# Performance work log

Measured on AMD Instinct MI355X. Metric: run time of the kernel, lower is better.

## Reference

```python
import jax, jax.numpy as jnp
import numpy as np

N_LEVELS = 16  # 2**4, bit = 4 in QuantLinear


def _sum_to(g, shape):
    # reduce grad g to broadcast shape `shape`
    extra = g.ndim - len(shape)
    if extra:
        g = g.sum(axis=tuple(range(extra)))
    axes = tuple(i for i, (gs, s) in enumerate(zip(g.shape, shape)) if s == 1 and gs != 1)
    if axes:
        g = g.sum(axis=axes, keepdims=True)
    return g.reshape(shape)


@jax.custom_vjp
def ste_round(x):
    return jnp.round(x)

def _r_fwd(x):
    return jnp.round(x), None

def _r_bwd(_, g):
    return (g,)

ste_round.defvjp(_r_fwd, _r_bwd)


@jax.custom_vjp
def dclip(x, lo, hi):
    return jnp.clip(x, lo, hi)

def _c_fwd(x, lo, hi):
    return jnp.clip(x, lo, hi), (x, lo, hi)

def _c_bwd(res, g):
    x, lo, hi = res
    gx = jnp.where((x < lo) | (x > hi), 0.0, g)
    glo = _sum_to(jnp.where(x > lo, 0.0, g), lo.shape)
    ghi = _sum_to(jnp.where(x < hi, 0.0, g), hi.shape)
    return gx, glo, ghi

dclip.defvjp(_c_fwd, _c_bwd)


def fake_quant(x, lb, ub):
    # UniformQuantizer.forward
    delta = (ub - lb) / (N_LEVELS - 1)
    x_cut = dclip(x, lb, ub)
    x_int = ste_round((x_cut - lb) / delta)
    return x_int * delta + lb


def setup_inputs() -> dict:
    key = jax.random.key(0)
    k0, k1, k2 = jax.random.split(key, 3)
    B, S, Din, Dout = 4, 4096, 1024, 3072
    x = jax.random.normal(k0, (B, S, Din), jnp.float32)
    weight = jax.random.normal(k1, (Dout, Din), jnp.float32) * 0.02
    bias = jax.random.normal(k2, (Dout,), jnp.float32) * 0.01
    # calibrated per-tensor activation bounds, per-output-channel weight bounds
    in_lb = jnp.full((1,), -2.5, jnp.float32)
    in_ub = jnp.full((1,), 2.5, jnp.float32)
    w_ub = jnp.max(jnp.abs(weight), axis=1, keepdims=True)  # (Dout, 1)
    w_lb = -w_ub
    return {"x": x, "weight": weight, "bias": bias,
            "in_lb": in_lb, "in_ub": in_ub, "w_lb": w_lb, "w_ub": w_ub}


def reference(x, weight, bias, in_lb, in_ub, w_lb, w_ub):
    qx = fake_quant(x, in_lb, in_ub)        # [B,S,Din]
    qw = fake_quant(weight, w_lb, w_ub)     # [Dout,Din]
    return jnp.einsum('bsi,oi->bso', qx, qw) + bias
```

## Files before the change

kernel.cpp:

```cpp
#include <hip/hip_runtime.h>

typedef int i32x4 __attribute__((ext_vector_type(4)));
typedef unsigned char u8x8 __attribute__((ext_vector_type(8)));


__global__ __launch_bounds__(512) void quant_i8_fused(
    const float* __restrict__ x, unsigned char* __restrict__ qx,
    float* __restrict__ Sx, const float* __restrict__ xlb,
    const float* __restrict__ xub, const float* __restrict__ w,
    unsigned char* __restrict__ qw, float* __restrict__ Sw,
    const float* __restrict__ wlb, const float* __restrict__ wub,
    int nxblocks) {
  const int tid = threadIdx.x;
  const int rloc = tid >> 7;
  const bool is_x = (int)blockIdx.x < nxblocks;
  const int rb = is_x ? blockIdx.x : blockIdx.x - nxblocks;
  const int row = rb * 4 + rloc;

  const float* src = is_x ? x : w;
  unsigned char* dst = is_x ? qx : qw;
  float* Sdst = is_x ? Sx : Sw;
  const float lb = is_x ? xlb[0] : wlb[row];
  const float ub = is_x ? xub[0] : wub[row];
  const float delta = (ub - lb) / 15.0f;

  const size_t base = (size_t)row * 1024 + (tid & 127) * 8;
  const float4* p = reinterpret_cast<const float4*>(src + base);
  float4 v0 = p[0], v1 = p[1];
  float vv[8] = {v0.x, v0.y, v0.z, v0.w, v1.x, v1.y, v1.z, v1.w};
  int s = 0;
  u8x8 o;
#pragma unroll
  for (int j = 0; j < 8; ++j) {
    float t = fminf(fmaxf(vv[j], lb), ub);
    int k = (int)rintf((t - lb) / delta);
    s += k;
    o[j] = (unsigned char)k;
  }
  *reinterpret_cast<u8x8*>(dst + base) = o;

#pragma unroll
  for (int d = 32; d > 0; d >>= 1) s += __shfl_down(s, d);
  __shared__ int wsum[8];
  if ((tid & 63) == 0) wsum[tid >> 6] = s;
  __syncthreads();
  if (tid < 4) Sdst[rb * 4 + tid] = (float)(wsum[2 * tid] + wsum[2 * tid + 1]);
}


__device__ __forceinline__ void gload_lds16(const unsigned char* g, unsigned char* l) {
  __builtin_amdgcn_global_load_lds(
      (const __attribute__((address_space(1))) unsigned int*)g,
      (__attribute__((address_space(3))) unsigned int*)l, 16, 0, 0);
}

#define SWZ(o) ((o) ^ ((((o) >> 7) & 3) << 4))

__global__ __launch_bounds__(512, 2) void gemm_i8_kernel(
    const unsigned char* __restrict__ A, const unsigned char* __restrict__ B,
    const float* __restrict__ bias, const float* __restrict__ Sx,
    const float* __restrict__ Sw, const float* __restrict__ wlb,
    const float* __restrict__ wub, const float* __restrict__ xlb,
    const float* __restrict__ xub, float* __restrict__ C, int M, int N) {
  const int K = 1024;
  const int NKT = 16;
  __shared__ unsigned char lds[3][24576];

  const int tid = threadIdx.x;
  const int w = tid >> 6, l = tid & 63;
  const int wm = w >> 1, wn = w & 1;

  int bid = blockIdx.x;
  { const int cpx = gridDim.x >> 3; bid = (bid & 7) * cpx + (bid >> 3); }
  const int ntn = N >> 7;
  const int tm = bid / ntn, tn = bid % ntn;

  const unsigned char* gA = A + (size_t)tm * 256 * K;
  const unsigned char* gB = B + (size_t)tn * 128 * K;

  const int p0 = tid * 16, p1 = 8192 + tid * 16, pB = tid * 16;
  const int o0 = SWZ(p0), o1 = SWZ(p1), oB = SWZ(pB);
  const unsigned char* sA0 = gA + (size_t)(o0 >> 6) * K + (o0 & 63);
  const unsigned char* sA1 = gA + (size_t)(o1 >> 6) * K + (o1 & 63);
  const unsigned char* sB0 = gB + (size_t)(oB >> 6) * K + (oB & 63);

  const int lroff = (l & 15) * 64 + (((l >> 4) * 16) ^ (((l >> 1) & 3) << 4));

#define STAGE_A(SB, KOFF) do {                                           \
    unsigned char* Rb_ = &lds[SB][0];                                    \
    gload_lds16(sA0 + (KOFF), Rb_ + p0);                                 \
    gload_lds16(sA1 + (KOFF), Rb_ + p1);                                 \
  } while (0)
#define STAGE_B(SB, KOFF) do {                                           \
    gload_lds16(sB0 + (KOFF), &lds[SB][16384] + pB);                     \
  } while (0)

#define RD_A(RB, F)  (*(const i32x4*)(&lds[RB][0]     + wm * 4096 + (F) * 1024 + lroff))
#define RD_B(RB, NN) (*(const i32x4*)(&lds[RB][16384] + wn * 4096 + (NN) * 1024 + lroff))

#define BAR __builtin_amdgcn_s_barrier()
#define LGKM0 do { asm volatile("s_waitcnt lgkmcnt(0)" ::: "memory");    \
                   __builtin_amdgcn_sched_barrier(0); } while (0)
#define VMC3 asm volatile("s_waitcnt vmcnt(3)" ::: "memory")

  i32x4 acc[4][4] = {};
  i32x4 av0, av1, av2, av3, bv[4];

#define MFMA_HALF(A0, A1, MH) do {                                       \
    __builtin_amdgcn_s_setprio(1);                                       \
    _Pragma("unroll") for (int nn = 0; nn < 4; ++nn)                     \
      acc[(MH) * 2 + 0][nn] = __builtin_amdgcn_mfma_i32_16x16x64_i8(     \
          A0, bv[nn], acc[(MH) * 2 + 0][nn], 0, 0, 0);                   \
    _Pragma("unroll") for (int nn = 0; nn < 4; ++nn)                     \
      acc[(MH) * 2 + 1][nn] = __builtin_amdgcn_mfma_i32_16x16x64_i8(     \
          A1, bv[nn], acc[(MH) * 2 + 1][nn], 0, 0, 0);                   \
    __builtin_amdgcn_s_setprio(0);                                       \
  } while (0)

  STAGE_A(0, 0); STAGE_B(0, 0);
  STAGE_A(1, 64); STAGE_B(1, 64);
  VMC3; BAR;

#pragma unroll
  for (int t = 0; t < NKT; ++t) {
    const int rb = t % 3, sb = (t + 2) % 3;
    const int koff = (t + 2 < NKT ? (t + 2) : 0) << 6;
    av0 = RD_A(rb, 0); av1 = RD_A(rb, 1);
#pragma unroll
    for (int nn = 0; nn < 4; ++nn) bv[nn] = RD_B(rb, nn);
    STAGE_A(sb, koff);
    BAR; LGKM0;
    MFMA_HALF(av0, av1, 0);
    BAR;
    av2 = RD_A(rb, 2); av3 = RD_A(rb, 3);
    STAGE_B(sb, koff);
    VMC3;
    BAR; LGKM0;
    MFMA_HALF(av2, av3, 1);
    BAR;
  }

  const float lbx = xlb[0];
  const float dx = (xub[0] - lbx) / 15.0f;
  const int rq = (l >> 4) * 4;
  const int cn = l & 15;
  const int mb = tm * 256 + wm * 64;
  const int nb = tn * 128 + wn * 64;

  float sxr[4][4];
#pragma unroll
  for (int m = 0; m < 4; ++m) {
    const int r0 = mb + m * 16 + rq;
#pragma unroll
    for (int j = 0; j < 4; ++j) sxr[m][j] = Sx[r0 + j];
  }
#pragma unroll
  for (int n = 0; n < 4; ++n) {
    const int col = nb + n * 16 + cn;
    const float wl = wlb[col], wu = wub[col];
    const float dw = (wu - wl) / 15.0f;
    const float c1 = dx * dw;
    const float c2 = dx * wl;
    const float c3 = lbx * dw * Sw[col] + 1024.0f * lbx * wl + bias[col];
#pragma unroll
    for (int m = 0; m < 4; ++m) {
      float* cp = C + (size_t)(mb + m * 16 + rq) * N + col;
      __builtin_nontemporal_store(c1 * (float)acc[m][n][0] + c2 * sxr[m][0] + c3, cp);
      __builtin_nontemporal_store(c1 * (float)acc[m][n][1] + c2 * sxr[m][1] + c3, cp + (size_t)N);
      __builtin_nontemporal_store(c1 * (float)acc[m][n][2] + c2 * sxr[m][2] + c3, cp + (size_t)2 * N);
      __builtin_nontemporal_store(c1 * (float)acc[m][n][3] + c2 * sxr[m][3] + c3, cp + (size_t)3 * N);
    }
  }
  asm volatile("s_waitcnt vmcnt(0)" ::: "memory");
#undef STAGE_A
#undef STAGE_B
#undef RD_A
#undef RD_B
#undef BAR
#undef LGKM0
#undef VMC3
#undef MFMA_HALF
}

extern "C" void kernel_launch(void* const* d_in, const int* in_sizes, int n_in,
                              void* d_out, int out_size, void* d_ws, size_t ws_size,
                              hipStream_t stream) {
  const float* x     = (const float*)d_in[0];
  const float* wgt   = (const float*)d_in[1];
  const float* bias  = (const float*)d_in[2];
  const float* in_lb = (const float*)d_in[3];
  const float* in_ub = (const float*)d_in[4];
  const float* w_lb  = (const float*)d_in[5];
  const float* w_ub  = (const float*)d_in[6];

  const int Dout = in_sizes[2];
  const int Din  = in_sizes[1] / Dout;
  const int M    = in_sizes[0] / Din;

  unsigned char* qx = (unsigned char*)d_ws;
  unsigned char* qw = qx + (size_t)M * Din;
  float* Sx = (float*)(qw + (size_t)Dout * Din);
  float* Sw = Sx + M;

  const int nxb = M / 4;
  quant_i8_fused<<<nxb + Dout / 4, 512, 0, stream>>>(
      x, qx, Sx, in_lb, in_ub, wgt, qw, Sw, w_lb, w_ub, nxb);

  dim3 grid((M / 256) * (Dout / 128));
  gemm_i8_kernel<<<grid, 512, 0, stream>>>(qx, qw, bias, Sx, Sw, w_lb, w_ub,
                                           in_lb, in_ub, (float*)d_out, M, Dout);
}
```

Measured before the change: 94.66 us.

## Shrink GEMM tile to 128x128 with 4 waves and load B directly into registers

The int8 GEMM moves from a 256x128 tile with 8 waves to a 128x128 tile with 4 waves and launch bounds of 3 blocks per CU. Only A is still staged through LDS in a triple buffer. Each wave now loads its B fragments straight from global memory into registers, double-buffered one k-step ahead. The goal is to cut LDS traffic and footprint and to simplify the per-k-step barrier schedule, in exchange for more grid blocks, redundant global reads of B across waves and tiles, and less A reuse per block.

Result: slower. 138.8 us (+46.7%).

```diff
diff --git a/kernel.cpp b/kernel.cpp
--- a/kernel.cpp
+++ b/kernel.cpp
@@ -2,7 +2,6 @@
 
 typedef int i32x4 __attribute__((ext_vector_type(4)));
 typedef unsigned char u8x8 __attribute__((ext_vector_type(8)));
-
 
 __global__ __launch_bounds__(512) void quant_i8_fused(
     const float* __restrict__ x, unsigned char* __restrict__ qx,
@@ -56,15 +55,14 @@
 
 #define SWZ(o) ((o) ^ ((((o) >> 7) & 3) << 4))
 
-__global__ __launch_bounds__(512, 2) void gemm_i8_kernel(
+__global__ __launch_bounds__(256, 3) void gemm_i8_kernel(
     const unsigned char* __restrict__ A, const unsigned char* __restrict__ B,
     const float* __restrict__ bias, const float* __restrict__ Sx,
     const float* __restrict__ Sw, const float* __restrict__ wlb,
     const float* __restrict__ wub, const float* __restrict__ xlb,
     const float* __restrict__ xub, float* __restrict__ C, int M, int N) {
   const int K = 1024;
-  const int NKT = 16;
-  __shared__ unsigned char lds[3][24576];
+  __shared__ unsigned char lds[3][8192];
 
   const int tid = threadIdx.x;
   const int w = tid >> 6, l = tid & 63;
@@ -75,76 +73,101 @@
   const int ntn = N >> 7;
   const int tm = bid / ntn, tn = bid % ntn;
 
-  const unsigned char* gA = A + (size_t)tm * 256 * K;
+  const unsigned char* gA = A + (size_t)tm * 128 * K;
   const unsigned char* gB = B + (size_t)tn * 128 * K;
 
-  const int p0 = tid * 16, p1 = 8192 + tid * 16, pB = tid * 16;
-  const int o0 = SWZ(p0), o1 = SWZ(p1), oB = SWZ(pB);
+  const int p0 = tid * 16, p1 = 4096 + tid * 16;
+  const int o0 = SWZ(p0), o1 = SWZ(p1);
   const unsigned char* sA0 = gA + (size_t)(o0 >> 6) * K + (o0 & 63);
   const unsigned char* sA1 = gA + (size_t)(o1 >> 6) * K + (o1 & 63);
-  const unsigned char* sB0 = gB + (size_t)(oB >> 6) * K + (oB & 63);
 
   const int lroff = (l & 15) * 64 + (((l >> 4) * 16) ^ (((l >> 1) & 3) << 4));
 
-#define STAGE_A(SB, KOFF) do {                                           \
+  const unsigned char* gB0 = gB + (size_t)(wn * 64 + (l & 15)) * K + (l >> 4) * 16;
+
+#define STAGE(SB, KOFF) do {                                             \
     unsigned char* Rb_ = &lds[SB][0];                                    \
     gload_lds16(sA0 + (KOFF), Rb_ + p0);                                 \
     gload_lds16(sA1 + (KOFF), Rb_ + p1);                                 \
   } while (0)
-#define STAGE_B(SB, KOFF) do {                                           \
-    gload_lds16(sB0 + (KOFF), &lds[SB][16384] + pB);                     \
+
+#define RD_A(RB, F) (*(const i32x4*)(&lds[RB][0] + wm * 4096 + (F) * 1024 + lroff))
+
+#define LOADB(D0, D1, D2, D3, T) do {                                    \
+    const int ko_ = ((T) < 16 ? (T) : 0) * 64;                           \
+    D0 = *(const i32x4*)(gB0 + ko_);                                     \
+    D1 = *(const i32x4*)(gB0 + 16 * 1024 + ko_);                         \
+    D2 = *(const i32x4*)(gB0 + 32 * 1024 + ko_);                         \
+    D3 = *(const i32x4*)(gB0 + 48 * 1024 + ko_);                         \
   } while (0)
 
-#define RD_A(RB, F)  (*(const i32x4*)(&lds[RB][0]     + wm * 4096 + (F) * 1024 + lroff))
-#define RD_B(RB, NN) (*(const i32x4*)(&lds[RB][16384] + wn * 4096 + (NN) * 1024 + lroff))
-
-#define BAR __builtin_amdgcn_s_barrier()
-#define LGKM0 do { asm volatile("s_waitcnt lgkmcnt(0)" ::: "memory");    \
-                   __builtin_amdgcn_sched_barrier(0); } while (0)
-#define VMC3 asm volatile("s_waitcnt vmcnt(3)" ::: "memory")
+#define SCB __builtin_amdgcn_sched_barrier(0)
+#define VMC0 do { asm volatile("s_waitcnt vmcnt(0)" ::: "memory"); SCB; } while (0)
+#define BARS do { __builtin_amdgcn_s_barrier(); SCB; } while (0)
 
   i32x4 acc[4][4] = {};
-  i32x4 av0, av1, av2, av3, bv[4];
-
-#define MFMA_HALF(A0, A1, MH) do {                                       \
+  i32x4 av0, av1, av2, av3;
+  i32x4 bc0, bc1, bc2, bc3, bn0, bn1, bn2, bn3;
+
+#define MF(AV, BV, CC) __builtin_amdgcn_mfma_i32_16x16x64_i8(AV, BV, CC, 0, 0, 0)
+
+#define TILE(T, C0, C1, C2, C3, N0, N1, N2, N3) do {                     \
+    av0 = RD_A((T) % 3, 0); av1 = RD_A((T) % 3, 1);                      \
+    av2 = RD_A((T) % 3, 2); av3 = RD_A((T) % 3, 3);                      \
+    LOADB(N0, N1, N2, N3, (T) + 1);                                      \
+    SCB;                                                                 \
     __builtin_amdgcn_s_setprio(1);                                       \
-    _Pragma("unroll") for (int nn = 0; nn < 4; ++nn)                     \
-      acc[(MH) * 2 + 0][nn] = __builtin_amdgcn_mfma_i32_16x16x64_i8(     \
-          A0, bv[nn], acc[(MH) * 2 + 0][nn], 0, 0, 0);                   \
-    _Pragma("unroll") for (int nn = 0; nn < 4; ++nn)                     \
-      acc[(MH) * 2 + 1][nn] = __builtin_amdgcn_mfma_i32_16x16x64_i8(     \
-          A1, bv[nn], acc[(MH) * 2 + 1][nn], 0, 0, 0);                   \
+    acc[0][0] = MF(av0, C0, acc[0][0]);                                  \
+    acc[0][1] = MF(av0, C1, acc[0][1]);                                  \
+    acc[0][2] = MF(av0, C2, acc[0][2]);                                  \
+    acc[0][3] = MF(av0, C3, acc[0][3]);                                  \
+    acc[1][0] = MF(av1, C0, acc[1][0]);                                  \
+    acc[1][1] = MF(av1, C1, acc[1][1]);                                  \
+    acc[1][2] = MF(av1, C2, acc[1][2]);                                  \
+    acc[1][3] = MF(av1, C3, acc[1][3]);                                  \
+    acc[2][0] = MF(av2, C0, acc[2][0]);                                  \
+    acc[2][1] = MF(av2, C1, acc[2][1]);                                  \
+    acc[2][2] = MF(av2, C2, acc[2][2]);                                  \
+    acc[2][3] = MF(av2, C3, acc[2][3]);                                  \
+    acc[3][0] = MF(av3, C0, acc[3][0]);                                  \
+    acc[3][1] = MF(av3, C1, acc[3][1]);                                  \
+    acc[3][2] = MF(av3, C2, acc[3][2]);                                  \
+    acc[3][3] = MF(av3, C3, acc[3][3]);                                  \
     __builtin_amdgcn_s_setprio(0);                                       \
+    VMC0; BARS;                                                          \
+    STAGE(((T) + 2) % 3, ((T) + 2 < 16 ? (T) + 2 : 0) * 64);             \
+    SCB;                                                                 \
   } while (0)
 
-  STAGE_A(0, 0); STAGE_B(0, 0);
-  STAGE_A(1, 64); STAGE_B(1, 64);
-  VMC3; BAR;
-
-#pragma unroll
-  for (int t = 0; t < NKT; ++t) {
-    const int rb = t % 3, sb = (t + 2) % 3;
-    const int koff = (t + 2 < NKT ? (t + 2) : 0) << 6;
-    av0 = RD_A(rb, 0); av1 = RD_A(rb, 1);
-#pragma unroll
-    for (int nn = 0; nn < 4; ++nn) bv[nn] = RD_B(rb, nn);
-    STAGE_A(sb, koff);
-    BAR; LGKM0;
-    MFMA_HALF(av0, av1, 0);
-    BAR;
-    av2 = RD_A(rb, 2); av3 = RD_A(rb, 3);
-    STAGE_B(sb, koff);
-    VMC3;
-    BAR; LGKM0;
-    MFMA_HALF(av2, av3, 1);
-    BAR;
-  }
+  STAGE(0, 0);
+  STAGE(1, 64);
+  LOADB(bc0, bc1, bc2, bc3, 0);
+  VMC0; BARS;
+
+  TILE(0,  bc0, bc1, bc2, bc3, bn0, bn1, bn2, bn3);
+  TILE(1,  bn0, bn1, bn2, bn3, bc0, bc1, bc2, bc3);
+  TILE(2,  bc0, bc1, bc2, bc3, bn0, bn1, bn2, bn3);
+  TILE(3,  bn0, bn1, bn2, bn3, bc0, bc1, bc2, bc3);
+  TILE(4,  bc0, bc1, bc2, bc3, bn0, bn1, bn2, bn3);
+  TILE(5,  bn0, bn1, bn2, bn3, bc0, bc1, bc2, bc3);
+  TILE(6,  bc0, bc1, bc2, bc3, bn0, bn1, bn2, bn3);
+  TILE(7,  bn0, bn1, bn2, bn3, bc0, bc1, bc2, bc3);
+  TILE(8,  bc0, bc1, bc2, bc3, bn0, bn1, bn2, bn3);
+  TILE(9,  bn0, bn1, bn2, bn3, bc0, bc1, bc2, bc3);
+  TILE(10, bc0, bc1, bc2, bc3, bn0, bn1, bn2, bn3);
+  TILE(11, bn0, bn1, bn2, bn3, bc0, bc1, bc2, bc3);
+  TILE(12, bc0, bc1, bc2, bc3, bn0, bn1, bn2, bn3);
+  TILE(13, bn0, bn1, bn2, bn3, bc0, bc1, bc2, bc3);
+  TILE(14, bc0, bc1, bc2, bc3, bn0, bn1, bn2, bn3);
+  TILE(15, bn0, bn1, bn2, bn3, bc0, bc1, bc2, bc3);
+
+  VMC0;
 
   const float lbx = xlb[0];
   const float dx = (xub[0] - lbx) / 15.0f;
   const int rq = (l >> 4) * 4;
   const int cn = l & 15;
-  const int mb = tm * 256 + wm * 64;
+  const int mb = tm * 128 + wm * 64;
   const int nb = tn * 128 + wn * 64;
 
   float sxr[4][4];
@@ -171,15 +194,14 @@
       __builtin_nontemporal_store(c1 * (float)acc[m][n][3] + c2 * sxr[m][3] + c3, cp + (size_t)3 * N);
     }
   }
-  asm volatile("s_waitcnt vmcnt(0)" ::: "memory");
-#undef STAGE_A
-#undef STAGE_B
+#undef STAGE
 #undef RD_A
-#undef RD_B
-#undef BAR
-#undef LGKM0
-#undef VMC3
-#undef MFMA_HALF
+#undef LOADB
+#undef SCB
+#undef VMC0
+#undef BARS
+#undef MF
+#undef TILE
 }
 
 extern "C" void kernel_launch(void* const* d_in, const int* in_sizes, int n_in,
@@ -206,7 +228,7 @@
   quant_i8_fused<<<nxb + Dout / 4, 512, 0, stream>>>(
       x, qx, Sx, in_lb, in_ub, wgt, qw, Sw, w_lb, w_ub, nxb);
 
-  dim3 grid((M / 256) * (Dout / 128));
-  gemm_i8_kernel<<<grid, 512, 0, stream>>>(qx, qw, bias, Sx, Sw, w_lb, w_ub,
+  dim3 grid((M / 128) * (Dout / 128));
+  gemm_i8_kernel<<<grid, 256, 0, stream>>>(qx, qw, bias, Sx, Sw, w_lb, w_ub,
                                            in_lb, in_ub, (float*)d_out, M, Dout);
 }
```

## Enlarge GEMM tile to 256x256 with double-buffered LDS pipeline

Applied to the files above, without the earlier changes.

The int8 GEMM block tile grows from 256x128 to 256x256, with each wave computing 128x64 outputs (32 accumulators) so every loaded A/B fragment is reused more. The LDS pipeline moves from three stages with split half-tiles and several barriers to two full-tile buffers, with one vmcnt(0) wait and one barrier per K step. The aim is to raise arithmetic intensity and cut synchronisation. In exchange, register pressure rises (128 accumulator VGPRs), the grid has half as many blocks, and global loads now overlap only one tile of compute.

Result: slower. 111.0 us (+17.3%).

```diff
diff --git a/kernel.cpp b/kernel.cpp
--- a/kernel.cpp
+++ b/kernel.cpp
@@ -2,7 +2,6 @@
 
 typedef int i32x4 __attribute__((ext_vector_type(4)));
 typedef unsigned char u8x8 __attribute__((ext_vector_type(8)));
-
 
 __global__ __launch_bounds__(512) void quant_i8_fused(
     const float* __restrict__ x, unsigned char* __restrict__ qx,
@@ -64,25 +63,26 @@
     const float* __restrict__ xub, float* __restrict__ C, int M, int N) {
   const int K = 1024;
   const int NKT = 16;
-  __shared__ unsigned char lds[3][24576];
+  __shared__ unsigned char lds[2][32768];
 
   const int tid = threadIdx.x;
   const int w = tid >> 6, l = tid & 63;
-  const int wm = w >> 1, wn = w & 1;
+  const int wm = w >> 2, wn = w & 3;
 
   int bid = blockIdx.x;
   { const int cpx = gridDim.x >> 3; bid = (bid & 7) * cpx + (bid >> 3); }
-  const int ntn = N >> 7;
+  const int ntn = N >> 8;
   const int tm = bid / ntn, tn = bid % ntn;
 
   const unsigned char* gA = A + (size_t)tm * 256 * K;
-  const unsigned char* gB = B + (size_t)tn * 128 * K;
-
-  const int p0 = tid * 16, p1 = 8192 + tid * 16, pB = tid * 16;
-  const int o0 = SWZ(p0), o1 = SWZ(p1), oB = SWZ(pB);
+  const unsigned char* gB = B + (size_t)tn * 256 * K;
+
+  const int p0 = tid * 16, p1 = 8192 + tid * 16;
+  const int o0 = SWZ(p0), o1 = SWZ(p1);
   const unsigned char* sA0 = gA + (size_t)(o0 >> 6) * K + (o0 & 63);
   const unsigned char* sA1 = gA + (size_t)(o1 >> 6) * K + (o1 & 63);
-  const unsigned char* sB0 = gB + (size_t)(oB >> 6) * K + (oB & 63);
+  const unsigned char* sB0 = gB + (size_t)(o0 >> 6) * K + (o0 & 63);
+  const unsigned char* sB1 = gB + (size_t)(o1 >> 6) * K + (o1 & 63);
 
   const int lroff = (l & 15) * 64 + (((l >> 4) * 16) ^ (((l >> 1) & 3) << 4));
 
@@ -92,68 +92,69 @@
     gload_lds16(sA1 + (KOFF), Rb_ + p1);                                 \
   } while (0)
 #define STAGE_B(SB, KOFF) do {                                           \
-    gload_lds16(sB0 + (KOFF), &lds[SB][16384] + pB);                     \
-  } while (0)
-
-#define RD_A(RB, F)  (*(const i32x4*)(&lds[RB][0]     + wm * 4096 + (F) * 1024 + lroff))
+    unsigned char* Rb_ = &lds[SB][16384];                                \
+    gload_lds16(sB0 + (KOFF), Rb_ + p0);                                 \
+    gload_lds16(sB1 + (KOFF), Rb_ + p1);                                 \
+  } while (0)
+
+#define RD_A(RB, F)  (*(const i32x4*)(&lds[RB][0]     + wm * 8192 + (F) * 1024 + lroff))
 #define RD_B(RB, NN) (*(const i32x4*)(&lds[RB][16384] + wn * 4096 + (NN) * 1024 + lroff))
 
-#define BAR __builtin_amdgcn_s_barrier()
+#define BARS do { __builtin_amdgcn_s_barrier();                          \
+                  __builtin_amdgcn_sched_barrier(0); } while (0)
 #define LGKM0 do { asm volatile("s_waitcnt lgkmcnt(0)" ::: "memory");    \
                    __builtin_amdgcn_sched_barrier(0); } while (0)
-#define VMC3 asm volatile("s_waitcnt vmcnt(3)" ::: "memory")
-
-  i32x4 acc[4][4] = {};
-  i32x4 av0, av1, av2, av3, bv[4];
-
-#define MFMA_HALF(A0, A1, MH) do {                                       \
+#define VMC0 do { asm volatile("s_waitcnt vmcnt(0)" ::: "memory");       \
+                  __builtin_amdgcn_sched_barrier(0); } while (0)
+
+  i32x4 acc[8][4] = {};
+  i32x4 av0, av1, av2, av3, av4, av5, av6, av7, bv0, bv1, bv2, bv3;
+
+#define MF(AV, BV, CC) __builtin_amdgcn_mfma_i32_16x16x64_i8(AV, BV, CC, 0, 0, 0)
+
+#define MROW(MI, AV) do {                                                \
+    acc[MI][0] = MF(AV, bv0, acc[MI][0]);                                \
+    acc[MI][1] = MF(AV, bv1, acc[MI][1]);                                \
+    acc[MI][2] = MF(AV, bv2, acc[MI][2]);                                \
+    acc[MI][3] = MF(AV, bv3, acc[MI][3]);                                \
+  } while (0)
+
+#define TILE(T) do {                                                     \
+    const int rb_ = (T) & 1, sb_ = ((T) + 1) & 1;                        \
+    const int ko_ = ((T) + 1 < NKT ? (T) + 1 : 0) << 6;                  \
+    av0 = RD_A(rb_, 0); av1 = RD_A(rb_, 1);                              \
+    av2 = RD_A(rb_, 2); av3 = RD_A(rb_, 3);                              \
+    bv0 = RD_B(rb_, 0); bv1 = RD_B(rb_, 1);                              \
+    bv2 = RD_B(rb_, 2); bv3 = RD_B(rb_, 3);                              \
+    STAGE_A(sb_, ko_);                                                   \
+    STAGE_B(sb_, ko_);                                                   \
+    LGKM0;                                                               \
     __builtin_amdgcn_s_setprio(1);                                       \
-    _Pragma("unroll") for (int nn = 0; nn < 4; ++nn)                     \
-      acc[(MH) * 2 + 0][nn] = __builtin_amdgcn_mfma_i32_16x16x64_i8(     \
-          A0, bv[nn], acc[(MH) * 2 + 0][nn], 0, 0, 0);                   \
-    _Pragma("unroll") for (int nn = 0; nn < 4; ++nn)                     \
-      acc[(MH) * 2 + 1][nn] = __builtin_amdgcn_mfma_i32_16x16x64_i8(     \
-          A1, bv[nn], acc[(MH) * 2 + 1][nn], 0, 0, 0);                   \
+    MROW(0, av0); MROW(1, av1); MROW(2, av2); MROW(3, av3);              \
     __builtin_amdgcn_s_setprio(0);                                       \
-  } while (0)
-
-  STAGE_A(0, 0); STAGE_B(0, 0);
-  STAGE_A(1, 64); STAGE_B(1, 64);
-  VMC3; BAR;
-
-#pragma unroll
-  for (int t = 0; t < NKT; ++t) {
-    const int rb = t % 3, sb = (t + 2) % 3;
-    const int koff = (t + 2 < NKT ? (t + 2) : 0) << 6;
-    av0 = RD_A(rb, 0); av1 = RD_A(rb, 1);
-#pragma unroll
-    for (int nn = 0; nn < 4; ++nn) bv[nn] = RD_B(rb, nn);
-    STAGE_A(sb, koff);
-    BAR; LGKM0;
-    MFMA_HALF(av0, av1, 0);
-    BAR;
-    av2 = RD_A(rb, 2); av3 = RD_A(rb, 3);
-    STAGE_B(sb, koff);
-    VMC3;
-    BAR; LGKM0;
-    MFMA_HALF(av2, av3, 1);
-    BAR;
-  }
+    av4 = RD_A(rb_, 4); av5 = RD_A(rb_, 5);                              \
+    av6 = RD_A(rb_, 6); av7 = RD_A(rb_, 7);                              \
+    LGKM0;                                                               \
+    __builtin_amdgcn_s_setprio(1);                                       \
+    MROW(4, av4); MROW(5, av5); MROW(6, av6); MROW(7, av7);              \
+    __builtin_amdgcn_s_setprio(0);                                       \
+    VMC0; BARS;                                                          \
+  } while (0)
+
+  STAGE_A(0, 0);
+  STAGE_B(0, 0);
+  VMC0; BARS;
+
+#pragma unroll
+  for (int t = 0; t < NKT; ++t) TILE(t);
 
   const float lbx = xlb[0];
   const float dx = (xub[0] - lbx) / 15.0f;
   const int rq = (l >> 4) * 4;
   const int cn = l & 15;
-  const int mb = tm * 256 + wm * 64;
-  const int nb = tn * 128 + wn * 64;
-
-  float sxr[4][4];
-#pragma unroll
-  for (int m = 0; m < 4; ++m) {
-    const int r0 = mb + m * 16 + rq;
-#pragma unroll
-    for (int j = 0; j < 4; ++j) sxr[m][j] = Sx[r0 + j];
-  }
+  const int mb = tm * 256 + wm * 128;
+  const int nb = tn * 256 + wn * 64;
+
 #pragma unroll
   for (int n = 0; n < 4; ++n) {
     const int col = nb + n * 16 + cn;
@@ -163,23 +164,25 @@
     const float c2 = dx * wl;
     const float c3 = lbx * dw * Sw[col] + 1024.0f * lbx * wl + bias[col];
 #pragma unroll
-    for (int m = 0; m < 4; ++m) {
-      float* cp = C + (size_t)(mb + m * 16 + rq) * N + col;
-      __builtin_nontemporal_store(c1 * (float)acc[m][n][0] + c2 * sxr[m][0] + c3, cp);
-      __builtin_nontemporal_store(c1 * (float)acc[m][n][1] + c2 * sxr[m][1] + c3, cp + (size_t)N);
-      __builtin_nontemporal_store(c1 * (float)acc[m][n][2] + c2 * sxr[m][2] + c3, cp + (size_t)2 * N);
-      __builtin_nontemporal_store(c1 * (float)acc[m][n][3] + c2 * sxr[m][3] + c3, cp + (size_t)3 * N);
+    for (int m = 0; m < 8; ++m) {
+      const int r0 = mb + m * 16 + rq;
+      float* cp = C + (size_t)r0 * N + col;
+      __builtin_nontemporal_store(c1 * (float)acc[m][n][0] + c2 * Sx[r0 + 0] + c3, cp);
+      __builtin_nontemporal_store(c1 * (float)acc[m][n][1] + c2 * Sx[r0 + 1] + c3, cp + (size_t)N);
+      __builtin_nontemporal_store(c1 * (float)acc[m][n][2] + c2 * Sx[r0 + 2] + c3, cp + (size_t)2 * N);
+      __builtin_nontemporal_store(c1 * (float)acc[m][n][3] + c2 * Sx[r0 + 3] + c3, cp + (size_t)3 * N);
     }
   }
-  asm volatile("s_waitcnt vmcnt(0)" ::: "memory");
 #undef STAGE_A
 #undef STAGE_B
 #undef RD_A
 #undef RD_B
-#undef BAR
+#undef BARS
 #undef LGKM0
-#undef VMC3
-#undef MFMA_HALF
+#undef VMC0
+#undef MF
+#undef MROW
+#undef TILE
 }
 
 extern "C" void kernel_launch(void* const* d_in, const int* in_sizes, int n_in,
@@ -206,7 +209,7 @@
   quant_i8_fused<<<nxb + Dout / 4, 512, 0, stream>>>(
       x, qx, Sx, in_lb, in_ub, wgt, qw, Sw, w_lb, w_ub, nxb);
 
-  dim3 grid((M / 256) * (Dout / 128));
+  dim3 grid((M / 256) * (Dout / 256));
   gemm_i8_kernel<<<grid, 512, 0, stream>>>(qx, qw, bias, Sx, Sw, w_lb, w_ub,
                                            in_lb, in_ub, (float*)d_out, M, Dout);
 }
```
